# Kernel tuning notes

Measured on AMD Instinct MI355X. Metric: run time of the kernel, lower is better.

Reference implementation:

```python
import jax, jax.numpy as jnp
import numpy as np

B, N, C, H = 2, 2048, 1024, 16
D = C // H
SCALE = D ** -0.5


def setup_inputs() -> dict:
    key = jax.random.key(0)
    ks = jax.random.split(key, 5)
    x = jax.random.normal(ks[0], (B, N, C), dtype=jnp.float32)
    # causal mask, broadcast over batch: True = attend
    attention_mask = jnp.broadcast_to(jnp.tril(jnp.ones((N, N), dtype=bool)), (B, N, N))
    w_qkv = jax.random.normal(ks[1], (3 * C, C), dtype=jnp.float32) * (C ** -0.5)
    b_qkv = jax.random.normal(ks[2], (3 * C,), dtype=jnp.float32) * 0.02
    w_proj = jax.random.normal(ks[3], (C, C), dtype=jnp.float32) * (C ** -0.5)
    b_proj = jax.random.normal(ks[4], (C,), dtype=jnp.float32) * 0.02
    return {"x": x, "attention_mask": attention_mask, "w_qkv": w_qkv,
            "b_qkv": b_qkv, "w_proj": w_proj, "b_proj": b_proj}


def reference(x, attention_mask, w_qkv, b_qkv, w_proj, b_proj):
    b, n, c = x.shape
    qkv = x @ w_qkv.T + b_qkv                      # [B,N,3C]
    qkv = qkv.reshape(b, n, 3, H, D).transpose(2, 0, 3, 1, 4)  # [3,B,H,N,D]
    q, k, v = qkv[0], qkv[1], qkv[2]
    dots = jnp.einsum('bhid,bhjd->bhij', q, k) * SCALE
    mask_value = -jnp.finfo(dots.dtype).max
    dots = jnp.where(attention_mask[:, None, :, :], dots, mask_value)
    attn = jax.nn.softmax(dots.astype(jnp.float32), axis=-1).astype(dots.dtype)
    out = jnp.einsum('bhij,bhjd->bhid', attn, v)   # [B,H,N,D]
    # NOTE: original code reshapes WITHOUT transposing heads back - faithful.
    out = out.reshape(b, n, c)
    return out @ w_proj.T + b_proj
```

## Files before the change

kernel.cpp:

```cpp
#include <hip/hip_runtime.h>
#include <hip/hip_bf16.h>
#include <stdint.h>

#define SL_F 0.18033688011112043f

typedef unsigned short u16;
typedef unsigned int u32;
typedef __attribute__((ext_vector_type(8))) short bf16x8;
typedef __attribute__((ext_vector_type(4))) float f32x4;

__device__ __forceinline__ u16 f2bf(float f) {
    union { float f; u32 u; } v; v.f = f;
    return (u16)((v.u + 0x7fffu + ((v.u >> 16) & 1u)) >> 16);
}
__device__ __forceinline__ u32 pack2bf(float a, float b) {
    union { __hip_bfloat162 h; u32 u; } p;
    p.h = __float22bfloat162_rn(make_float2(a, b));
    return p.u;
}

__device__ __forceinline__ void gl_lds16(const u16* g, u16* l) {
    __builtin_amdgcn_global_load_lds(
        (const __attribute__((address_space(1))) u32*)g,
        (__attribute__((address_space(3))) u32*)l, 16, 0, 0);
}

__global__ __launch_bounds__(256) void convert_k(
    const float* __restrict__ x, const float* __restrict__ w1,
    const float* __restrict__ w2,
    u16* __restrict__ xb, u16* __restrict__ w1b, u16* __restrict__ w2b)
{
    const int t = blockIdx.x * 256 + threadIdx.x;
    const int XA = 524288, XW1 = 393216;
    const float* src; u16* dst; int s;
    if (t < XA)            { src = x;  dst = xb;  s = t; }
    else if (t < XA + XW1) { src = w1; dst = w1b; s = t - XA; }
    else                   { src = w2; dst = w2b; s = t - XA - XW1; }
    const int c = s >> 6;
    const int u = s & 63;
    const int l = (u >> 2) + 16 * (u & 3);
    const int g = c >> 5, kb = c & 31;
    const int row = g * 16 + (l & 15);
    const int k0 = kb * 32 + (l >> 4) * 8;
    const float4 v0 = *(const float4*)&src[(size_t)row * 1024 + k0];
    const float4 v1 = *(const float4*)&src[(size_t)row * 1024 + k0 + 4];
    uint4 o;
    o.x = pack2bf(v0.x, v0.y); o.y = pack2bf(v0.z, v0.w);
    o.z = pack2bf(v1.x, v1.y); o.w = pack2bf(v1.z, v1.w);
    *(uint4*)&dst[((size_t)c * 64 + l) * 8] = o;
}

__global__ __launch_bounds__(256) void qkv_gemm(
    const u16* __restrict__ A, const u16* __restrict__ Bw,
    const float* __restrict__ bias,
    u16* __restrict__ Qb, u16* __restrict__ Kb, u16* __restrict__ VTb)
{
    __shared__ __align__(16) u16 Al[2][8 * 512];
    __shared__ __align__(16) u16 Bl[2][8 * 512];
    const int tid = threadIdx.x;
    const int lane = tid & 63;
    const int w = tid >> 6;
    const int la = lane & 15, qd = lane >> 4;
    const int m0 = blockIdx.y * 128;
    const int n0 = blockIdx.x * 128;
    const int wm = (w >> 1) * 64, wn = (w & 1) * 64;

    const u16* Ag0 = A + ((size_t)((m0 >> 4) + 2 * w) * 32) * 512 + lane * 8;
    const u16* Ag1 = Ag0 + 32 * 512;
    const u16* Bg0 = Bw + ((size_t)((n0 >> 4) + 2 * w) * 32) * 512 + lane * 8;
    const u16* Bg1 = Bg0 + 32 * 512;

    auto stage = [&](int k0, int b) {
        const size_t ko = (size_t)(k0 >> 5) * 512;
        gl_lds16(Ag0 + ko, &Al[b][(2 * w) * 512]);
        gl_lds16(Ag1 + ko, &Al[b][(2 * w + 1) * 512]);
        gl_lds16(Bg0 + ko, &Bl[b][(2 * w) * 512]);
        gl_lds16(Bg1 + ko, &Bl[b][(2 * w + 1) * 512]);
    };

    f32x4 acc[4][4] = {};
    int buf = 0;
    stage(0, 0);

    for (int k0 = 0; k0 < 1024; k0 += 32) {
        __syncthreads();
        if (k0 + 32 < 1024) stage(k0 + 32, buf ^ 1);

        bf16x8 af[4], bfr[4];
#pragma unroll
        for (int i = 0; i < 4; i++)
            af[i] = *(const bf16x8*)&Al[buf][(((unsigned)wm >> 4) + i) * 512 + lane * 8];
#pragma unroll
        for (int j = 0; j < 4; j++)
            bfr[j] = *(const bf16x8*)&Bl[buf][(((unsigned)wn >> 4) + j) * 512 + lane * 8];
#pragma unroll
        for (int i = 0; i < 4; i++)
#pragma unroll
            for (int j = 0; j < 4; j++)
                acc[i][j] = __builtin_amdgcn_mfma_f32_16x16x32_bf16(
                    af[i], bfr[j], acc[i][j], 0, 0, 0);
        buf ^= 1;
    }

#pragma unroll
    for (int j = 0; j < 4; j++) {
        const int col = n0 + wn + j * 16 + la;
        const float bv = bias[col];
        const int t = col >> 10, hd = col & 1023, h = hd >> 6, d = hd & 63;
#pragma unroll
        for (int i = 0; i < 4; i++)
#pragma unroll
            for (int r = 0; r < 4; r++) {
                const int row = m0 + wm + i * 16 + qd * 4 + r;
                const int b = row >> 11, n = row & 2047;
                const int bh = b * 16 + h;
                const u16 val = f2bf(acc[i][j][r] + bv);
                if (t == 0)      Qb[((size_t)bh * 2048 + n) * 64 + d] = val;
                else if (t == 1) Kb[((size_t)bh * 2048 + n) * 64 + d] = val;
                else             VTb[((size_t)bh * 64 + d) * 2048 + n] = val;
            }
    }
}

__global__ __launch_bounds__(256) void proj_gemm(
    const u16* __restrict__ A, const u16* __restrict__ Bw,
    const float* __restrict__ bias, float* __restrict__ Out)
{
    __shared__ __align__(16) u16 Al[2][16 * 512];
    __shared__ __align__(16) u16 Bl[2][8 * 512];
    const int tid = threadIdx.x;
    const int lane = tid & 63;
    const int w = tid >> 6;
    const int la = lane & 15, qd = lane >> 4;
    const int K = 1024;
    const int m0 = blockIdx.y * 128;
    const int n0 = blockIdx.x * 64;
    const int wm = (w >> 1) * 64, wn = (w & 1) * 32;

    const u16* Asrc[4];
#pragma unroll
    for (int t = 0; t < 4; t++) {
        const int ck = 4 * w + t, g = ck >> 1, h = ck & 1;
        Asrc[t] = A + (size_t)(m0 + g * 16 + la) * K + h * 32 + qd * 8;
    }
    const u16* Bg = Bw + ((size_t)((n0 >> 4) + w) * 32) * 512 + lane * 8;

    auto stage = [&](int k0, int b) {
#pragma unroll
        for (int t = 0; t < 4; t++)
            gl_lds16(Asrc[t] + k0, &Al[b][(4 * w + t) * 512]);
#pragma unroll
        for (int t = 0; t < 2; t++)
            gl_lds16(Bg + (size_t)((k0 >> 5) + t) * 512, &Bl[b][(2 * w + t) * 512]);
    };

    f32x4 acc[4][2] = {};
    int buf = 0;
    stage(0, 0);

    for (int k0 = 0; k0 < K; k0 += 64) {
        __syncthreads();
        if (k0 + 64 < K) stage(k0 + 64, buf ^ 1);

        bf16x8 af[4][2], bfr[2][2];
#pragma unroll
        for (int i = 0; i < 4; i++) {
            const int g = ((unsigned)wm >> 4) + i;
#pragma unroll
            for (int h = 0; h < 2; h++)
                af[i][h] = *(const bf16x8*)&Al[buf][(g * 2 + h) * 512 + lane * 8];
        }
#pragma unroll
        for (int j = 0; j < 2; j++) {
            const int g = ((unsigned)wn >> 4) + j;
#pragma unroll
            for (int h = 0; h < 2; h++)
                bfr[j][h] = *(const bf16x8*)&Bl[buf][(g * 2 + h) * 512 + lane * 8];
        }
#pragma unroll
        for (int i = 0; i < 4; i++)
#pragma unroll
            for (int j = 0; j < 2; j++) {
                f32x4 c = acc[i][j];
                c = __builtin_amdgcn_mfma_f32_16x16x32_bf16(af[i][0], bfr[j][0], c, 0, 0, 0);
                c = __builtin_amdgcn_mfma_f32_16x16x32_bf16(af[i][1], bfr[j][1], c, 0, 0, 0);
                acc[i][j] = c;
            }
        buf ^= 1;
    }

#pragma unroll
    for (int j = 0; j < 2; j++) {
        const int col = n0 + wn + j * 16 + la;
        const float bv = bias[col];
#pragma unroll
        for (int i = 0; i < 4; i++)
#pragma unroll
            for (int r = 0; r < 4; r++) {
                const int row = m0 + wm + i * 16 + qd * 4 + r;
                Out[(size_t)row * 1024 + col] = acc[i][j][r] + bv;
            }
    }
}

__global__ __launch_bounds__(256) void attn_k(
    const u16* __restrict__ Qb, const u16* __restrict__ Kb,
    const u16* __restrict__ VTb, u16* __restrict__ Ob)
{
    __shared__ __align__(16) u16 Kl[2][16 * 512];
    __shared__ __align__(16) u16 Vl[2][16 * 512];
    __shared__ __align__(16) u16 Pl[4][16 * 72];
    const int bh = blockIdx.x & 31;
    const int pair = blockIdx.x >> 5;
    const int tid = threadIdx.x;
    const int lane = tid & 63;
    const int w = tid >> 6;
    const int la = lane & 15, qd = lane >> 4;

    const u16* Kbase = Kb + (size_t)bh * 2048 * 64;
    const u16* Vbase = VTb + (size_t)bh * 64 * 2048;
    u16* Pw = &Pl[w][0];

    u32 ksrc[4], vsrc[4];
#pragma unroll
    for (int t = 0; t < 4; t++) {
        const int ck = 4 * w + t;
        ksrc[t] = (u32)((ck >> 1) * 16 + la) * 64 + (ck & 1) * 32 + qd * 8;
        vsrc[t] = (u32)((ck >> 2) * 16 + la) * 2048 + (ck & 3) * 32 + qd * 8;
    }
    auto stage = [&](int j0, int b) {
#pragma unroll
        for (int t = 0; t < 4; t++) {
            gl_lds16(Kbase + (u32)j0 * 64 + ksrc[t], &Kl[b][(4 * w + t) * 512]);
            gl_lds16(Vbase + (u32)j0 + vsrc[t], &Vl[b][(4 * w + t) * 512]);
        }
    };

    int buf = 0;
    stage(0, 0);

    for (int half = 0; half < 2; half++) {
        const int tile = (half == 0) ? pair : 31 - pair;
        const int q0 = tile * 64 + w * 16;
        const int jmax = (tile >> 1) * 128;
        const int qrow = q0 + la;

        const u16* Qp = Qb + ((size_t)bh * 2048 + q0 + la) * 64 + qd * 8;
        const bf16x8 qf0 = *(const bf16x8*)Qp;
        const bf16x8 qf1 = *(const bf16x8*)(Qp + 32);

        f32x4 o[4] = {};
        float lsum = 0.f;

        for (int j0 = 0; j0 <= jmax; j0 += 128) {
            __syncthreads();

            const int nj = (j0 + 128 <= jmax) ? (j0 + 128) : ((half == 0) ? 0 : -1);
            if (nj >= 0) stage(nj, buf ^ 1);

            f32x4 s[8];
#pragma unroll
            for (int c = 0; c < 8; c++) {
                f32x4 z = {};
                const bf16x8 kf0 = *(const bf16x8*)&Kl[buf][(c * 2 + 0) * 512 + lane * 8];
                const bf16x8 kf1 = *(const bf16x8*)&Kl[buf][(c * 2 + 1) * 512 + lane * 8];
                z = __builtin_amdgcn_mfma_f32_16x16x32_bf16(kf0, qf0, z, 0, 0, 0);
                z = __builtin_amdgcn_mfma_f32_16x16x32_bf16(kf1, qf1, z, 0, 0, 0);
                s[c] = z;
            }

            if (j0 == jmax) {
#pragma unroll
                for (int c = 0; c < 8; c++)
#pragma unroll
                    for (int r = 0; r < 4; r++) {
                        const int j = j0 + c * 16 + qd * 4 + r;
                        float v = s[c][r] * SL_F;
                        v = (j > qrow) ? -1e30f : v;
                        s[c][r] = __builtin_amdgcn_exp2f(v);
                    }
            } else {
#pragma unroll
                for (int c = 0; c < 8; c++)
#pragma unroll
                    for (int r = 0; r < 4; r++)
                        s[c][r] = __builtin_amdgcn_exp2f(s[c][r] * SL_F);
            }
#pragma unroll
            for (int c = 0; c < 8; c++)
#pragma unroll
                for (int r = 0; r < 4; r++)
                    lsum += s[c][r];

#pragma unroll
            for (int hh = 0; hh < 2; hh++) {
#pragma unroll
                for (int c = 0; c < 4; c++) {
                    uint2 pw;
                    pw.x = pack2bf(s[hh * 4 + c][0], s[hh * 4 + c][1]);
                    pw.y = pack2bf(s[hh * 4 + c][2], s[hh * 4 + c][3]);
                    *(uint2*)&Pw[la * 72 + c * 16 + qd * 4] = pw;
                }
                const bf16x8 pf0 = *(const bf16x8*)&Pw[la * 72 + qd * 8];
                const bf16x8 pf1 = *(const bf16x8*)&Pw[la * 72 + 32 + qd * 8];
#pragma unroll
                for (int c2 = 0; c2 < 4; c2++) {
                    const bf16x8 vf0 = *(const bf16x8*)&Vl[buf][(c2 * 4 + hh * 2 + 0) * 512 + lane * 8];
                    const bf16x8 vf1 = *(const bf16x8*)&Vl[buf][(c2 * 4 + hh * 2 + 1) * 512 + lane * 8];
                    o[c2] = __builtin_amdgcn_mfma_f32_16x16x32_bf16(pf0, vf0, o[c2], 0, 0, 0);
                    o[c2] = __builtin_amdgcn_mfma_f32_16x16x32_bf16(pf1, vf1, o[c2], 0, 0, 0);
                }
            }
            buf ^= 1;
        }

        lsum += __shfl_xor(lsum, 16, 64);
        lsum += __shfl_xor(lsum, 32, 64);
        float rinv[4];
#pragma unroll
        for (int r = 0; r < 4; r++)
            rinv[r] = 1.0f / __shfl(lsum, qd * 4 + r, 64);

        u16* Op = Ob + (size_t)bh * 2048 * 64;
#pragma unroll
        for (int c2 = 0; c2 < 4; c2++)
#pragma unroll
            for (int r = 0; r < 4; r++) {
                const int row = q0 + qd * 4 + r;
                Op[(size_t)row * 64 + c2 * 16 + la] = f2bf(o[c2][r] * rinv[r]);
            }
    }
}

extern "C" void kernel_launch(void* const* d_in, const int* in_sizes, int n_in,
                              void* d_out, int out_size, void* d_ws, size_t ws_size,
                              hipStream_t stream)
{
    const float* x     = (const float*)d_in[0];
    const float* wqkv  = (const float*)d_in[2];
    const float* bqkv  = (const float*)d_in[3];
    const float* wproj = (const float*)d_in[4];
    const float* bproj = (const float*)d_in[5];
    float* out = (float*)d_out;

    u16* ws     = (u16*)d_ws;
    u16* xb     = ws;
    u16* wqkvb  = xb + 4096 * 1024;
    u16* wprojb = wqkvb + 3072 * 1024;
    u16* Qb     = wprojb + 1024 * 1024;
    u16* Kb     = Qb + 32 * 2048 * 64;
    u16* VTb    = Kb + 32 * 2048 * 64;
    u16* Ob     = VTb + 32 * 2048 * 64;

    convert_k<<<dim3(4096), dim3(256), 0, stream>>>(
        x, wqkv, wproj, xb, wqkvb, wprojb);

    qkv_gemm<<<dim3(24, 32), dim3(256), 0, stream>>>(
        xb, wqkvb, bqkv, Qb, Kb, VTb);

    attn_k<<<dim3(512), dim3(256), 0, stream>>>(Qb, Kb, VTb, Ob);

    proj_gemm<<<dim3(16, 32), dim3(256), 0, stream>>>(
        Ob, wprojb, bproj, out);
}
```

Measured before the change: 209.2 us.

## Store K, V^T and attention output in pre-tiled MFMA fragment layout

The QKV GEMM epilogue now writes K and V^T, and the attention kernel writes its output, directly in a tiled 512-element-chunk layout that matches the LDS fragment order. The global-to-LDS async loads in the attention and projection kernels then become contiguous 1 KB chunk copies with lane*8 addressing instead of strided row gathers. This is meant to cut uncoalesced global reads and address arithmetic, at the cost of more scattered scalar stores in the epilogues.

Measured after the change: 212.1 us. No clear change (+1.4%).

```diff
diff --git a/kernel.cpp b/kernel.cpp
--- a/kernel.cpp
+++ b/kernel.cpp
@@ -115,9 +115,14 @@
                 const int b = row >> 11, n = row & 2047;
                 const int bh = b * 16 + h;
                 const u16 val = f2bf(acc[i][j][r] + bv);
-                if (t == 0)      Qb[((size_t)bh * 2048 + n) * 64 + d] = val;
-                else if (t == 1) Kb[((size_t)bh * 2048 + n) * 64 + d] = val;
-                else             VTb[((size_t)bh * 64 + d) * 2048 + n] = val;
+                if (t == 0)
+                    Qb[((size_t)bh * 2048 + n) * 64 + d] = val;
+                else if (t == 1)
+                    Kb[((size_t)bh * 256 + (n >> 4) * 2 + (d >> 5)) * 512
+                       + ((n & 15) + 16 * ((d >> 3) & 3)) * 8 + (d & 7)] = val;
+                else
+                    VTb[((size_t)bh * 256 + (n >> 7) * 16 + (d >> 4) * 4 + ((n >> 5) & 3)) * 512
+                        + ((d & 15) + 16 * ((n >> 3) & 3)) * 8 + (n & 7)] = val;
             }
     }
 }
@@ -137,18 +142,18 @@
     const int n0 = blockIdx.x * 64;
     const int wm = (w >> 1) * 64, wn = (w & 1) * 32;
 
-    const u16* Asrc[4];
+    const u16* Ab[4];
 #pragma unroll
     for (int t = 0; t < 4; t++) {
         const int ck = 4 * w + t, g = ck >> 1, h = ck & 1;
-        Asrc[t] = A + (size_t)(m0 + g * 16 + la) * K + h * 32 + qd * 8;
+        Ab[t] = A + (((size_t)(m0 >> 4) + g) * 32 + h) * 512 + lane * 8;
     }
     const u16* Bg = Bw + ((size_t)((n0 >> 4) + w) * 32) * 512 + lane * 8;
 
     auto stage = [&](int k0, int b) {
 #pragma unroll
         for (int t = 0; t < 4; t++)
-            gl_lds16(Asrc[t] + k0, &Al[b][(4 * w + t) * 512]);
+            gl_lds16(Ab[t] + (size_t)(k0 >> 5) * 512, &Al[b][(4 * w + t) * 512]);
 #pragma unroll
         for (int t = 0; t < 2; t++)
             gl_lds16(Bg + (size_t)((k0 >> 5) + t) * 512, &Bl[b][(2 * w + t) * 512]);
@@ -217,22 +222,16 @@
     const int w = tid >> 6;
     const int la = lane & 15, qd = lane >> 4;
 
-    const u16* Kbase = Kb + (size_t)bh * 2048 * 64;
-    const u16* Vbase = VTb + (size_t)bh * 64 * 2048;
+    const u16* Kbh = Kb + (size_t)bh * 256 * 512 + lane * 8;
+    const u16* Vbh = VTb + (size_t)bh * 256 * 512 + lane * 8;
     u16* Pw = &Pl[w][0];
 
-    u32 ksrc[4], vsrc[4];
-#pragma unroll
-    for (int t = 0; t < 4; t++) {
-        const int ck = 4 * w + t;
-        ksrc[t] = (u32)((ck >> 1) * 16 + la) * 64 + (ck & 1) * 32 + qd * 8;
-        vsrc[t] = (u32)((ck >> 2) * 16 + la) * 2048 + (ck & 3) * 32 + qd * 8;
-    }
     auto stage = [&](int j0, int b) {
 #pragma unroll
         for (int t = 0; t < 4; t++) {
-            gl_lds16(Kbase + (u32)j0 * 64 + ksrc[t], &Kl[b][(4 * w + t) * 512]);
-            gl_lds16(Vbase + (u32)j0 + vsrc[t], &Vl[b][(4 * w + t) * 512]);
+            const int ck = 4 * w + t;
+            gl_lds16(Kbh + (size_t)((j0 >> 3) + ck) * 512, &Kl[b][ck * 512]);
+            gl_lds16(Vbh + (size_t)((j0 >> 7) * 16 + ck) * 512, &Vl[b][ck * 512]);
         }
     };
 
@@ -321,13 +320,17 @@
         for (int r = 0; r < 4; r++)
             rinv[r] = 1.0f / __shfl(lsum, qd * 4 + r, 64);
 
-        u16* Op = Ob + (size_t)bh * 2048 * 64;
+        const int m = bh * 128 + (q0 >> 4);
+        u16* Ot = Ob + ((size_t)(m >> 4) * 32) * 512;
+        const int mm = m & 15;
 #pragma unroll
         for (int c2 = 0; c2 < 4; c2++)
 #pragma unroll
             for (int r = 0; r < 4; r++) {
-                const int row = q0 + qd * 4 + r;
-                Op[(size_t)row * 64 + c2 * 16 + la] = f2bf(o[c2][r] * rinv[r]);
+                const int kk5 = (qd * 4 + r) * 2 + (c2 >> 1);
+                const int s3 = (c2 * 2 + (la >> 3)) & 3;
+                Ot[(size_t)kk5 * 512 + (mm + 16 * s3) * 8 + (la & 7)] =
+                    f2bf(o[c2][r] * rinv[r]);
             }
     }
 }
```
